# Kernel optimization log

Measured on AMD Instinct MI355X. Metric: run time of the kernel, lower is better.

Reference implementation:

```python
import jax, jax.numpy as jnp
import numpy as np
import math

LOG2PI = math.log(2.0 * math.pi)


def _gm_scale(m1, v1, m2, v2):
    # log-scale of product of two diagonal Gaussians (summed over last dim D)
    v1s = jnp.exp(2.0 * v1)
    v2s = jnp.exp(2.0 * v2)
    s = v1s + v2s
    ls = jnp.log(s)
    return (-0.5 * (LOG2PI + ls + (m1 - m2) ** 2 / s)).sum(-1)


def _gm_full(m1, v1, m2, v2):
    v1s = jnp.exp(2.0 * v1)
    v2s = jnp.exp(2.0 * v2)
    s = v1s + v2s
    ls = jnp.log(s)
    scale = (-0.5 * (LOG2PI + ls + (m1 - m2) ** 2 / s)).sum(-1)
    mu = (m1 * v2s + m2 * v1s) / s
    var = v1 + v2 - 0.5 * ls
    return scale, mu, var


def _child_part(cw, cm, cv, t_mu, t_var, side):
    # cw: (M,L,K); cm/cv: (M,L,K,D); t_mu/t_var: (L,L,L,C,D)
    if side == 'left':
        cm_b = cm[:, None, :, None, None, :, :]
        cv_b = cv[:, None, :, None, None, :, :]
        cw_b = cw[:, None, :, None, None, :]
    else:
        cm_b = cm[:, None, None, :, None, :, :]
        cv_b = cv[:, None, None, :, None, :, :]
        cw_b = cw[:, None, None, :, None, :]
    t_mu_b = t_mu[None, :, :, :, :, None, :]
    t_var_b = t_var[None, :, :, :, :, None, :]
    scale = _gm_scale(cm_b, cv_b, t_mu_b, t_var_b)  # (M,L,L,L,C,K)
    return jax.nn.logsumexp(scale + cw_b, axis=-1)  # (M,L,L,L,C)


def setup_inputs() -> dict:
    key = jax.random.key(0)
    ks = jax.random.split(key, 10)
    L, C, Ks, D = 5, 4, 4, 4
    n_leaves = 128
    N = 2 * n_leaves - 1  # complete binary tree, level order, leaves first
    f = jax.random.normal
    return {
        'state_weight': f(ks[0], (N, L, Ks), jnp.float32) * 0.5,
        'state_mu': f(ks[1], (N, L, Ks, D), jnp.float32) * 0.5,
        'state_var': f(ks[2], (N, L, Ks, D), jnp.float32) * 0.1,
        'trans_weight': f(ks[3], (L, L, L, C), jnp.float32) * 0.5,
        'trans_mu_p': f(ks[4], (L, L, L, C, D), jnp.float32) * 0.5,
        'trans_mu_lc': f(ks[5], (L, L, L, C, D), jnp.float32) * 0.5,
        'trans_mu_rc': f(ks[6], (L, L, L, C, D), jnp.float32) * 0.5,
        'trans_var_p': f(ks[7], (L, L, L, C, D), jnp.float32) * 0.1,
        'trans_var_lc': f(ks[8], (L, L, L, C, D), jnp.float32) * 0.1,
        'trans_var_rc': f(ks[9], (L, L, L, C, D), jnp.float32) * 0.1,
        'n_leaves': n_leaves,
    }


def reference(state_weight, state_mu, state_var, trans_weight, trans_mu_p,
              trans_mu_lc, trans_mu_rc, trans_var_p, trans_var_lc,
              trans_var_rc, n_leaves):
    L = trans_weight.shape[0]
    D = trans_mu_p.shape[-1]
    # inside pass over a complete binary tree, level by level
    w = state_weight[:n_leaves]      # (M,L,K)
    mu = state_mu[:n_leaves]         # (M,L,K,D)
    var = state_var[:n_leaves]
    off = n_leaves
    m = n_leaves // 2
    while m >= 1:
        left = _child_part(w[0::2], mu[0::2], var[0::2], trans_mu_lc, trans_var_lc, 'left')
        right = _child_part(w[1::2], mu[1::2], var[1::2], trans_mu_rc, trans_var_rc, 'right')
        cs = left + right + trans_weight[None]  # (m,L,L,L,C)
        sw = state_weight[off:off + m]          # (m,L,Ks)
        sm = state_mu[off:off + m]
        sv = state_var[off:off + m]
        sm_b = sm[:, :, None, None, :, None, :]   # (m,L,1,1,Ks,1,D)
        sv_b = sv[:, :, None, None, :, None, :]
        tp_mu = trans_mu_p[None, :, :, :, None, :, :]   # (1,L,L,L,1,C,D)
        tp_var = trans_var_p[None, :, :, :, None, :, :]
        scale, pmu, pvar = _gm_full(sm_b, sv_b, tp_mu, tp_var)  # (m,L,L,L,Ks,C)
        score = scale + cs[:, :, :, :, None, :] + sw[:, :, None, None, :, None]
        w = score.reshape(m, L, -1)  # K = L*L*Ks*C
        mu = jnp.broadcast_to(pmu, score.shape + (D,)).reshape(m, L, -1, D)
        var = jnp.broadcast_to(pvar, score.shape + (D,)).reshape(m, L, -1, D)
        off += m
        m //= 2
    return w[0], mu[0], var[0]
```

## Files before the change

### kernel.cpp

```cpp
#include <hip/hip_runtime.h>
#include <math.h>

#define L2PI4      7.3515082656373812f
#define HALF_L2PI4 3.6757541328186906f
#define LOG2E      1.4426950408889634f
#define LN2        0.6931471805599453f
#define C_HQ       0.7213475204444817f

__device__ __forceinline__ float frcp(float x)  { return __builtin_amdgcn_rcpf(x); }
__device__ __forceinline__ float frsq(float x)  { return __builtin_amdgcn_rsqf(x); }
__device__ __forceinline__ float flog2(float x) { return __builtin_amdgcn_logf(x); }
__device__ __forceinline__ float fexp2(float x) { return __builtin_amdgcn_exp2f(x); }

__global__ __launch_bounds__(256) void kL1(
    const float* __restrict__ sw, const float* __restrict__ smu,
    const float* __restrict__ svar,
    const float4* __restrict__ tmL4, const float4* __restrict__ tvL4,
    const float4* __restrict__ tmR4, const float4* __restrict__ tvR4,
    const float* __restrict__ tvarp, const float* __restrict__ tvarl,
    const float* __restrict__ tvarr,
    float* __restrict__ tveP, float* __restrict__ tveL, float* __restrict__ tveR,
    float* __restrict__ lr)
{
    int cn = blockIdx.x, side = cn & 1, tid = threadIdx.x;
    if (cn < 24) {
        int t = cn >> 3;
        int base = (cn & 7) * 250;
        const float* src = (t == 0) ? tvarp : (t == 1) ? tvarl : tvarr;
        float* dst       = (t == 0) ? tveP  : (t == 1) ? tveL  : tveR;
        for (int i = tid; i < 250; i += 256)
            dst[base + i] = __expf(2.f * src[base + i]);
    }
    __shared__ float s_cm[80], s_cve[80], s_cw2[20];
    if (tid < 80) {
        s_cm[tid]  = smu[cn * 80 + tid];
        s_cve[tid] = __expf(2.f * svar[cn * 80 + tid]);
        if (tid < 20) s_cw2[tid] = (sw[cn * 20 + tid] - HALF_L2PI4) * LOG2E;
    }
    __syncthreads();
    const float4* tm = side ? tmR4 : tmL4;
    const float4* tv = side ? tvR4 : tvL4;
    for (int e = tid; e < 500; e += 256) {
        int c = e & 3, r = e >> 2;
        int lo = r % 5, r2 = r / 5, lp = r2 % 5, lc2 = r2 / 5;
        int idx = side ? (((lp * 5 + lo) * 5 + lc2) * 4 + c)
                       : (((lp * 5 + lc2) * 5 + lo) * 4 + c);
        float4 tmo = tm[idx];
        float4 tvr = tv[idx];
        float4 tvo = make_float4(__expf(2.f * tvr.x), __expf(2.f * tvr.y),
                                 __expf(2.f * tvr.z), __expf(2.f * tvr.w));
        float vals[4];
        #pragma unroll
        for (int k = 0; k < 4; ++k) {
            int ci = (lc2 * 4 + k) * 4;
            float s0 = s_cve[ci+0] + tvo.x, s1 = s_cve[ci+1] + tvo.y;
            float s2 = s_cve[ci+2] + tvo.z, s3 = s_cve[ci+3] + tvo.w;
            float d0 = s_cm[ci+0] - tmo.x, d1 = s_cm[ci+1] - tmo.y;
            float d2 = s_cm[ci+2] - tmo.z, d3 = s_cm[ci+3] - tmo.w;
            float p01 = s0 * s1, p23 = s2 * s3;
            float q01 = fmaf(d0 * d0, s1, d1 * d1 * s0);
            float q23 = fmaf(d2 * d2, s3, d3 * d3 * s2);
            float P = p01 * p23;
            float Q = fmaf(q01, p23, q23 * p01);
            float rq = frsq(P);
            float QP = Q * rq * rq;
            vals[k] = fmaf(-0.5f, flog2(P), fmaf(-C_HQ, QP, s_cw2[lc2 * 4 + k]));
        }
        float M = fmaxf(fmaxf(vals[0], vals[1]), fmaxf(vals[2], vals[3]));
        float S = fexp2(vals[0]-M) + fexp2(vals[1]-M)
                + fexp2(vals[2]-M) + fexp2(vals[3]-M);
        lr[(size_t)cn * 500 + idx] = (M + flog2(S)) * LN2;
    }
}

__global__ __launch_bounds__(256) void kAB(
    const float* __restrict__ lrP, float* __restrict__ lrC,
    const float* __restrict__ sw, const float* __restrict__ smu,
    const float* __restrict__ svar, int childOff,
    const float* __restrict__ tw, const float4* __restrict__ tmp4,
    const float4* __restrict__ tep4,
    const float4* __restrict__ tmL4, const float4* __restrict__ tveL4,
    const float4* __restrict__ tmR4, const float4* __restrict__ tveR4,
    int log2m)
{
    int bid = blockIdx.x;
    int p = bid & ((1 << log2m) - 1), sl = bid >> log2m;
    int side = (sl >= 25) ? 1 : 0;
    int r0 = sl - side * 25;
    int lc = r0 / 5, lp = r0 - lc * 5;
    int tid = threadIdx.x, lane = tid & 63, wave = tid >> 6;
    int cn = 2 * p + side;
    int node = childOff + cn;

    __shared__ float  s_sm[16], s_sve[16], s_swl[4];
    __shared__ float4 s_fm[400], s_fv[400];
    __shared__ float  s_fw[400];
    __shared__ float4 s_tm[20], s_tv[20];
    __shared__ int    s_idx[20];

    if (tid < 16) {
        s_sm[tid]  = smu[node * 80 + lc * 16 + tid];
        s_sve[tid] = __expf(2.f * svar[node * 80 + lc * 16 + tid]);
        if (tid < 4) s_swl[tid] = sw[node * 20 + lc * 4 + tid];
    }
    {
        const float4* tmf  = side ? tmR4  : tmL4;
        const float4* tvef = side ? tveR4 : tveL4;
        if (tid >= 64 && tid < 84) {
            int o = tid - 64, lo = o >> 2, c = o & 3;
            int idx = side ? (((lp * 5 + lo) * 5 + lc) * 4 + c)
                           : (((lp * 5 + lc) * 5 + lo) * 4 + c);
            s_idx[o] = idx;
            s_tm[o]  = tmf[idx];
            s_tv[o]  = tvef[idx];
        }
    }
    __syncthreads();

    const float* lrL = lrP + (size_t)(2 * cn) * 500;
    const float* lrR = lrP + (size_t)(2 * cn + 1) * 500;

    for (int e = tid; e < 400; e += 256) {
        int c2 = e & 3, ks = (e >> 2) & 3, r = e >> 4;
        int t4 = (lc * 25 + r) * 4 + c2;
        float csv = lrL[t4] + lrR[t4] + tw[t4];
        float4 m2 = tmp4[t4], e2 = tep4[t4];
        float base2 = (csv + s_swl[ks] - L2PI4) * LOG2E;
        float v0 = s_sve[ks*4+0], v1 = s_sve[ks*4+1];
        float v2 = s_sve[ks*4+2], v3 = s_sve[ks*4+3];
        float m10 = s_sm[ks*4+0], m11 = s_sm[ks*4+1];
        float m12 = s_sm[ks*4+2], m13 = s_sm[ks*4+3];
        float s0 = v0 + e2.x, s1 = v1 + e2.y, s2 = v2 + e2.z, s3 = v3 + e2.w;
        float rs0 = frcp(s0), rs1 = frcp(s1), rs2 = frcp(s2), rs3 = frcp(s3);
        float d0 = m10 - m2.x, d1 = m11 - m2.y, d2 = m12 - m2.z, d3 = m13 - m2.w;
        float qs = fmaf(d0 * d0, rs0, fmaf(d1 * d1, rs1,
                   fmaf(d2 * d2, rs2, d3 * d3 * rs3)));
        float P = (s0 * s1) * (s2 * s3);
        float4 fm, fv;
        fm.x = fmaf(m10, e2.x, m2.x * v0) * rs0;  fv.x = v0 * e2.x * rs0;
        fm.y = fmaf(m11, e2.y, m2.y * v1) * rs1;  fv.y = v1 * e2.y * rs1;
        fm.z = fmaf(m12, e2.z, m2.z * v2) * rs2;  fv.z = v2 * e2.z * rs2;
        fm.w = fmaf(m13, e2.w, m2.w * v3) * rs3;  fv.w = v3 * e2.w * rs3;
        s_fm[e] = fm;
        s_fv[e] = fv;
        s_fw[e] = fmaf(-0.5f, flog2(P), fmaf(-C_HQ, qs, base2));
    }
    __syncthreads();

    float E[7], M;
    {
        float w[7];
        #pragma unroll
        for (int i = 0; i < 7; ++i) {
            int k = lane + (i << 6);
            int kc = k < 400 ? k : 0;
            w[i] = (k < 400) ? s_fw[kc] : -1e30f;
        }
        M = w[0];
        #pragma unroll
        for (int i = 1; i < 7; ++i) M = fmaxf(M, w[i]);
        #pragma unroll
        for (int s = 32; s; s >>= 1) M = fmaxf(M, __shfl_xor(M, s));
        #pragma unroll
        for (int i = 0; i < 7; ++i) E[i] = fexp2(w[i] - M);
    }

    size_t lrb = (size_t)cn * 500;
    #pragma unroll
    for (int j = 0; j < 5; ++j) {
        int o = wave + 4 * j;
        float4 tmo = s_tm[o], tvo = s_tv[o];
        float S = 0.f;
        #pragma unroll
        for (int i = 0; i < 7; ++i) {
            int k = lane + (i << 6);
            int kc = k < 400 ? k : 0;
            float4 fm = s_fm[kc], fv = s_fv[kc];
            float ss0 = fv.x + tvo.x, ss1 = fv.y + tvo.y;
            float ss2 = fv.z + tvo.z, ss3 = fv.w + tvo.w;
            float dd0 = fm.x - tmo.x, dd1 = fm.y - tmo.y;
            float dd2 = fm.z - tmo.z, dd3 = fm.w - tmo.w;
            float p01 = ss0 * ss1, p23 = ss2 * ss3;
            float q01 = fmaf(dd0 * dd0, ss1, dd1 * dd1 * ss0);
            float q23 = fmaf(dd2 * dd2, ss3, dd3 * dd3 * ss2);
            float P = p01 * p23;
            float Q = fmaf(q01, p23, q23 * p01);
            float rq = frsq(P);
            float QP = Q * rq * rq;
            S = fmaf(E[i] * rq, fexp2(-C_HQ * QP), S);
        }
        #pragma unroll
        for (int s = 32; s; s >>= 1) S += __shfl_xor(S, s);
        if (lane == 0) lrC[lrb + s_idx[o]] = (M + flog2(S)) * LN2;
    }
}

__global__ __launch_bounds__(256) void kFin(
    const float* __restrict__ lrC,
    const float* __restrict__ sw, const float* __restrict__ smu,
    const float* __restrict__ svar, int rootNode,
    const float* __restrict__ tw, const float4* __restrict__ tmp4,
    const float4* __restrict__ tvp4, const float4* __restrict__ tep4,
    float* __restrict__ outw, float4* __restrict__ outmu4,
    float4* __restrict__ outvar4)
{
    int e = blockIdx.x * 256 + threadIdx.x;
    if (e >= 2000) return;
    int c = e & 3, ks = (e >> 2) & 3, r = e >> 4;
    int lrc = r % 5, r2 = r / 5, llc = r2 % 5, lp = r2 / 5;
    int t4 = ((lp * 5 + llc) * 5 + lrc) * 4 + c;
    float csv = lrC[t4] + lrC[500 + t4] + tw[t4];
    float4 m2 = tmp4[t4], v2 = tvp4[t4], e2 = tep4[t4];
    int sb = rootNode * 80 + (lp * 4 + ks) * 4;
    float base = csv + sw[rootNode * 20 + lp * 4 + ks] - HALF_L2PI4;
    float scale = 0.f;
    float4 pmu, pvar;
    {
        float m1 = smu[sb+0], v1 = svar[sb+0], v1s = __expf(2.f * v1);
        float s = v1s + e2.x, rs = frcp(s), ls = flog2(s) * LN2, df = m1 - m2.x;
        scale += ls + df * df * rs;
        pmu.x = fmaf(m1, e2.x, m2.x * v1s) * rs; pvar.x = v1 + v2.x - 0.5f * ls;
    }
    {
        float m1 = smu[sb+1], v1 = svar[sb+1], v1s = __expf(2.f * v1);
        float s = v1s + e2.y, rs = frcp(s), ls = flog2(s) * LN2, df = m1 - m2.y;
        scale += ls + df * df * rs;
        pmu.y = fmaf(m1, e2.y, m2.y * v1s) * rs; pvar.y = v1 + v2.y - 0.5f * ls;
    }
    {
        float m1 = smu[sb+2], v1 = svar[sb+2], v1s = __expf(2.f * v1);
        float s = v1s + e2.z, rs = frcp(s), ls = flog2(s) * LN2, df = m1 - m2.z;
        scale += ls + df * df * rs;
        pmu.z = fmaf(m1, e2.z, m2.z * v1s) * rs; pvar.z = v1 + v2.z - 0.5f * ls;
    }
    {
        float m1 = smu[sb+3], v1 = svar[sb+3], v1s = __expf(2.f * v1);
        float s = v1s + e2.w, rs = frcp(s), ls = flog2(s) * LN2, df = m1 - m2.w;
        scale += ls + df * df * rs;
        pmu.w = fmaf(m1, e2.w, m2.w * v1s) * rs; pvar.w = v1 + v2.w - 0.5f * ls;
    }
    outw[e]    = fmaf(-0.5f, scale, base);
    outmu4[e]  = pmu;
    outvar4[e] = pvar;
}

extern "C" void kernel_launch(void* const* d_in, const int* in_sizes, int n_in,
                              void* d_out, int out_size, void* d_ws, size_t ws_size,
                              hipStream_t stream) {
    (void)in_sizes; (void)n_in; (void)out_size; (void)ws_size;
    const float* sw      = (const float*)d_in[0];
    const float* smu     = (const float*)d_in[1];
    const float* svar    = (const float*)d_in[2];
    const float* tw      = (const float*)d_in[3];
    const float* tmu_p   = (const float*)d_in[4];
    const float* tmu_lc  = (const float*)d_in[5];
    const float* tmu_rc  = (const float*)d_in[6];
    const float* tvar_p  = (const float*)d_in[7];
    const float* tvar_lc = (const float*)d_in[8];
    const float* tvar_rc = (const float*)d_in[9];

    float* ws   = (float*)d_ws;
    float* lrA  = ws;
    float* lrB  = lrA + 64000;
    float* tveP = lrB + 64000;
    float* tveL = tveP + 2000;
    float* tveR = tveL + 2000;
    float* out  = (float*)d_out;

    hipLaunchKernelGGL(kL1, dim3(128), dim3(256), 0, stream,
                       sw, smu, svar,
                       (const float4*)tmu_lc, (const float4*)tvar_lc,
                       (const float4*)tmu_rc, (const float4*)tvar_rc,
                       tvar_p, tvar_lc, tvar_rc,
                       tveP, tveL, tveR, lrA);

    const int childOffs[6] = {128, 192, 224, 240, 248, 252};
    float* lrP = lrA;
    float* lrC = lrB;
    int li = 0;
    for (int lg = 5; lg >= 0; --lg, ++li) {
        int m = 1 << lg;
        hipLaunchKernelGGL(kAB, dim3(50 * m), dim3(256), 0, stream,
                           lrP, lrC,
                           sw, smu, svar, childOffs[li],
                           tw, (const float4*)tmu_p, (const float4*)tveP,
                           (const float4*)tmu_lc, (const float4*)tveL,
                           (const float4*)tmu_rc, (const float4*)tveR,
                           lg);
        float* t = lrP; lrP = lrC; lrC = t;
    }
    hipLaunchKernelGGL(kFin, dim3(8), dim3(256), 0, stream,
                       lrP, sw, smu, svar, 254,
                       tw, (const float4*)tmu_p, (const float4*)tvar_p,
                       (const float4*)tveP,
                       out, (float4*)(out + 2000), (float4*)(out + 10000));
}
```

Baseline: 65.89 us.

## Fuse leaf-level lr computation into first tree level and final step into last

Removes the separate leaf kernel by having the first level kernel recompute both children's leaf log-responsibilities in shared memory. It also drops the precomputed exp(2*var) tables in favour of inline exponentials, and folds the final root kernel into the last level through an atomic last-block-done counter. Net effect: two fewer kernel launches plus a memset, in exchange for redundant leaf recomputation across the 25 lc/lp blocks that share each child pair and extra exp work.

Result: slower. 72.39 us (+9.9%).

```diff
diff --git a/kernel.cpp b/kernel.cpp
--- a/kernel.cpp
+++ b/kernel.cpp
@@ -12,119 +12,105 @@
 __device__ __forceinline__ float flog2(float x) { return __builtin_amdgcn_logf(x); }
 __device__ __forceinline__ float fexp2(float x) { return __builtin_amdgcn_exp2f(x); }
 
-__global__ __launch_bounds__(256) void kL1(
+__global__ __launch_bounds__(256) void kAB32(
     const float* __restrict__ sw, const float* __restrict__ smu,
     const float* __restrict__ svar,
+    const float* __restrict__ tw, const float4* __restrict__ tmp4,
+    const float4* __restrict__ tvp4,
     const float4* __restrict__ tmL4, const float4* __restrict__ tvL4,
     const float4* __restrict__ tmR4, const float4* __restrict__ tvR4,
-    const float* __restrict__ tvarp, const float* __restrict__ tvarl,
-    const float* __restrict__ tvarr,
-    float* __restrict__ tveP, float* __restrict__ tveL, float* __restrict__ tveR,
-    float* __restrict__ lr)
+    float* __restrict__ lrC)
 {
-    int cn = blockIdx.x, side = cn & 1, tid = threadIdx.x;
-    if (cn < 24) {
-        int t = cn >> 3;
-        int base = (cn & 7) * 250;
-        const float* src = (t == 0) ? tvarp : (t == 1) ? tvarl : tvarr;
-        float* dst       = (t == 0) ? tveP  : (t == 1) ? tveL  : tveR;
-        for (int i = tid; i < 250; i += 256)
-            dst[base + i] = __expf(2.f * src[base + i]);
-    }
-    __shared__ float s_cm[80], s_cve[80], s_cw2[20];
-    if (tid < 80) {
-        s_cm[tid]  = smu[cn * 80 + tid];
-        s_cve[tid] = __expf(2.f * svar[cn * 80 + tid]);
-        if (tid < 20) s_cw2[tid] = (sw[cn * 20 + tid] - HALF_L2PI4) * LOG2E;
-    }
-    __syncthreads();
-    const float4* tm = side ? tmR4 : tmL4;
-    const float4* tv = side ? tvR4 : tvL4;
-    for (int e = tid; e < 500; e += 256) {
-        int c = e & 3, r = e >> 2;
-        int lo = r % 5, r2 = r / 5, lp = r2 % 5, lc2 = r2 / 5;
-        int idx = side ? (((lp * 5 + lo) * 5 + lc2) * 4 + c)
-                       : (((lp * 5 + lc2) * 5 + lo) * 4 + c);
-        float4 tmo = tm[idx];
-        float4 tvr = tv[idx];
+    int bid = blockIdx.x;
+    int p = bid & 31, sl = bid >> 5;
+    int side = (sl >= 25) ? 1 : 0;
+    int r0 = sl - side * 25;
+    int lc = r0 / 5, lp = r0 - lc * 5;
+    int tid = threadIdx.x, lane = tid & 63, wave = tid >> 6;
+    int cn = 2 * p + side;
+    int node = 128 + cn;
+
+    __shared__ float  s_lm[160], s_lve[160], s_lw2[40];
+    __shared__ float  s_lr[200];
+    __shared__ float  s_sm[16], s_sve[16], s_swl[4];
+    __shared__ float4 s_fm[400], s_fv[400];
+    __shared__ float  s_fw[400];
+    __shared__ float4 s_tm[20], s_tv[20];
+    __shared__ int    s_idx[20];
+
+    if (tid < 160) {
+        int which = tid >= 80, i = tid - which * 80;
+        int nl = 2 * cn + which;
+        s_lm[tid]  = smu[nl * 80 + i];
+        s_lve[tid] = __expf(2.f * svar[nl * 80 + i]);
+    } else if (tid < 200) {
+        int t = tid - 160, which = t >= 20, i = t - which * 20;
+        int nl = 2 * cn + which;
+        s_lw2[t] = (sw[nl * 20 + i] - HALF_L2PI4) * LOG2E;
+    } else if (tid < 216) {
+        int i = tid - 200;
+        s_sm[i]  = smu[node * 80 + lc * 16 + i];
+        s_sve[i] = __expf(2.f * svar[node * 80 + lc * 16 + i]);
+    } else if (tid < 220) {
+        s_swl[tid - 216] = sw[node * 20 + lc * 4 + (tid - 216)];
+    } else if (tid < 240) {
+        int o = tid - 220, lo = o >> 2, c = o & 3;
+        int idx = side ? (((lp * 5 + lo) * 5 + lc) * 4 + c)
+                       : (((lp * 5 + lc) * 5 + lo) * 4 + c);
+        s_idx[o] = idx;
+        const float4* tmf = side ? tmR4 : tmL4;
+        const float4* tvf = side ? tvR4 : tvL4;
+        s_tm[o] = tmf[idx];
+        float4 tvr = tvf[idx];
+        s_tv[o] = make_float4(__expf(2.f * tvr.x), __expf(2.f * tvr.y),
+                              __expf(2.f * tvr.z), __expf(2.f * tvr.w));
+    }
+    __syncthreads();
+
+    for (int t = tid; t < 200; t += 256) {
+        int which = t >= 100, q = t - which * 100;
+        int r = q >> 2, c2 = q & 3;
+        int llc = r / 5, lrc = r - llc * 5;
+        int t4 = (lc * 25 + r) * 4 + c2;
+        int lab = which ? lrc : llc;
+        float4 tm  = (which ? tmR4 : tmL4)[t4];
+        float4 tvr = (which ? tvR4 : tvL4)[t4];
         float4 tvo = make_float4(__expf(2.f * tvr.x), __expf(2.f * tvr.y),
                                  __expf(2.f * tvr.z), __expf(2.f * tvr.w));
+        int sb = which * 80 + lab * 16;
         float vals[4];
         #pragma unroll
         for (int k = 0; k < 4; ++k) {
-            int ci = (lc2 * 4 + k) * 4;
-            float s0 = s_cve[ci+0] + tvo.x, s1 = s_cve[ci+1] + tvo.y;
-            float s2 = s_cve[ci+2] + tvo.z, s3 = s_cve[ci+3] + tvo.w;
-            float d0 = s_cm[ci+0] - tmo.x, d1 = s_cm[ci+1] - tmo.y;
-            float d2 = s_cm[ci+2] - tmo.z, d3 = s_cm[ci+3] - tmo.w;
+            int ci = sb + k * 4;
+            float s0 = s_lve[ci+0] + tvo.x, s1 = s_lve[ci+1] + tvo.y;
+            float s2 = s_lve[ci+2] + tvo.z, s3 = s_lve[ci+3] + tvo.w;
+            float d0 = s_lm[ci+0] - tm.x, d1 = s_lm[ci+1] - tm.y;
+            float d2 = s_lm[ci+2] - tm.z, d3 = s_lm[ci+3] - tm.w;
             float p01 = s0 * s1, p23 = s2 * s3;
             float q01 = fmaf(d0 * d0, s1, d1 * d1 * s0);
             float q23 = fmaf(d2 * d2, s3, d3 * d3 * s2);
             float P = p01 * p23;
             float Q = fmaf(q01, p23, q23 * p01);
             float rq = frsq(P);
-            float QP = Q * rq * rq;
-            vals[k] = fmaf(-0.5f, flog2(P), fmaf(-C_HQ, QP, s_cw2[lc2 * 4 + k]));
+            vals[k] = fmaf(-0.5f, flog2(P),
+                           fmaf(-C_HQ, Q * rq * rq, s_lw2[which * 20 + lab * 4 + k]));
         }
         float M = fmaxf(fmaxf(vals[0], vals[1]), fmaxf(vals[2], vals[3]));
         float S = fexp2(vals[0]-M) + fexp2(vals[1]-M)
                 + fexp2(vals[2]-M) + fexp2(vals[3]-M);
-        lr[(size_t)cn * 500 + idx] = (M + flog2(S)) * LN2;
-    }
-}
-
-__global__ __launch_bounds__(256) void kAB(
-    const float* __restrict__ lrP, float* __restrict__ lrC,
-    const float* __restrict__ sw, const float* __restrict__ smu,
-    const float* __restrict__ svar, int childOff,
-    const float* __restrict__ tw, const float4* __restrict__ tmp4,
-    const float4* __restrict__ tep4,
-    const float4* __restrict__ tmL4, const float4* __restrict__ tveL4,
-    const float4* __restrict__ tmR4, const float4* __restrict__ tveR4,
-    int log2m)
-{
-    int bid = blockIdx.x;
-    int p = bid & ((1 << log2m) - 1), sl = bid >> log2m;
-    int side = (sl >= 25) ? 1 : 0;
-    int r0 = sl - side * 25;
-    int lc = r0 / 5, lp = r0 - lc * 5;
-    int tid = threadIdx.x, lane = tid & 63, wave = tid >> 6;
-    int cn = 2 * p + side;
-    int node = childOff + cn;
-
-    __shared__ float  s_sm[16], s_sve[16], s_swl[4];
-    __shared__ float4 s_fm[400], s_fv[400];
-    __shared__ float  s_fw[400];
-    __shared__ float4 s_tm[20], s_tv[20];
-    __shared__ int    s_idx[20];
-
-    if (tid < 16) {
-        s_sm[tid]  = smu[node * 80 + lc * 16 + tid];
-        s_sve[tid] = __expf(2.f * svar[node * 80 + lc * 16 + tid]);
-        if (tid < 4) s_swl[tid] = sw[node * 20 + lc * 4 + tid];
-    }
-    {
-        const float4* tmf  = side ? tmR4  : tmL4;
-        const float4* tvef = side ? tveR4 : tveL4;
-        if (tid >= 64 && tid < 84) {
-            int o = tid - 64, lo = o >> 2, c = o & 3;
-            int idx = side ? (((lp * 5 + lo) * 5 + lc) * 4 + c)
-                           : (((lp * 5 + lc) * 5 + lo) * 4 + c);
-            s_idx[o] = idx;
-            s_tm[o]  = tmf[idx];
-            s_tv[o]  = tvef[idx];
-        }
-    }
-    __syncthreads();
-
-    const float* lrL = lrP + (size_t)(2 * cn) * 500;
-    const float* lrR = lrP + (size_t)(2 * cn + 1) * 500;
+        s_lr[t] = (M + flog2(S)) * LN2;
+    }
+    __syncthreads();
 
     for (int e = tid; e < 400; e += 256) {
         int c2 = e & 3, ks = (e >> 2) & 3, r = e >> 4;
+        int q = r * 4 + c2;
         int t4 = (lc * 25 + r) * 4 + c2;
-        float csv = lrL[t4] + lrR[t4] + tw[t4];
-        float4 m2 = tmp4[t4], e2 = tep4[t4];
+        float csv = s_lr[q] + s_lr[100 + q] + tw[t4];
+        float4 m2 = tmp4[t4];
+        float4 vr = tvp4[t4];
+        float4 e2 = make_float4(__expf(2.f * vr.x), __expf(2.f * vr.y),
+                                __expf(2.f * vr.z), __expf(2.f * vr.w));
         float base2 = (csv + s_swl[ks] - L2PI4) * LOG2E;
         float v0 = s_sve[ks*4+0], v1 = s_sve[ks*4+1];
         float v2 = s_sve[ks*4+2], v3 = s_sve[ks*4+3];
@@ -153,8 +139,7 @@
         #pragma unroll
         for (int i = 0; i < 7; ++i) {
             int k = lane + (i << 6);
-            int kc = k < 400 ? k : 0;
-            w[i] = (k < 400) ? s_fw[kc] : -1e30f;
+            w[i] = (k < 400) ? s_fw[k] : -1e30f;
         }
         M = w[0];
         #pragma unroll
@@ -164,7 +149,6 @@
         #pragma unroll
         for (int i = 0; i < 7; ++i) E[i] = fexp2(w[i] - M);
     }
-
     size_t lrb = (size_t)cn * 500;
     #pragma unroll
     for (int j = 0; j < 5; ++j) {
@@ -186,8 +170,7 @@
             float P = p01 * p23;
             float Q = fmaf(q01, p23, q23 * p01);
             float rq = frsq(P);
-            float QP = Q * rq * rq;
-            S = fmaf(E[i] * rq, fexp2(-C_HQ * QP), S);
+            S = fmaf(E[i] * rq, fexp2(-C_HQ * (Q * rq * rq)), S);
         }
         #pragma unroll
         for (int s = 32; s; s >>= 1) S += __shfl_xor(S, s);
@@ -195,53 +178,183 @@
     }
 }
 
-__global__ __launch_bounds__(256) void kFin(
-    const float* __restrict__ lrC,
+__global__ __launch_bounds__(256) void kAB(
+    const float* __restrict__ lrP, float* __restrict__ lrC,
     const float* __restrict__ sw, const float* __restrict__ smu,
-    const float* __restrict__ svar, int rootNode,
+    const float* __restrict__ svar, int childOff,
     const float* __restrict__ tw, const float4* __restrict__ tmp4,
-    const float4* __restrict__ tvp4, const float4* __restrict__ tep4,
-    float* __restrict__ outw, float4* __restrict__ outmu4,
-    float4* __restrict__ outvar4)
+    const float4* __restrict__ tvp4,
+    const float4* __restrict__ tmL4, const float4* __restrict__ tvL4,
+    const float4* __restrict__ tmR4, const float4* __restrict__ tvR4,
+    int log2m, int doFin, unsigned* __restrict__ cnt, float* __restrict__ out)
 {
-    int e = blockIdx.x * 256 + threadIdx.x;
-    if (e >= 2000) return;
-    int c = e & 3, ks = (e >> 2) & 3, r = e >> 4;
-    int lrc = r % 5, r2 = r / 5, llc = r2 % 5, lp = r2 / 5;
-    int t4 = ((lp * 5 + llc) * 5 + lrc) * 4 + c;
-    float csv = lrC[t4] + lrC[500 + t4] + tw[t4];
-    float4 m2 = tmp4[t4], v2 = tvp4[t4], e2 = tep4[t4];
-    int sb = rootNode * 80 + (lp * 4 + ks) * 4;
-    float base = csv + sw[rootNode * 20 + lp * 4 + ks] - HALF_L2PI4;
-    float scale = 0.f;
-    float4 pmu, pvar;
+    int bid = blockIdx.x;
+    int p = bid & ((1 << log2m) - 1), sl = bid >> log2m;
+    int side = (sl >= 25) ? 1 : 0;
+    int r0 = sl - side * 25;
+    int lc = r0 / 5, lp = r0 - lc * 5;
+    int tid = threadIdx.x, lane = tid & 63, wave = tid >> 6;
+    int cn = 2 * p + side;
+    int node = childOff + cn;
+
+    __shared__ float  s_sm[16], s_sve[16], s_swl[4];
+    __shared__ float4 s_fm[400], s_fv[400];
+    __shared__ float  s_fw[400];
+    __shared__ float4 s_tm[20], s_tv[20];
+    __shared__ int    s_idx[20];
+    __shared__ int    s_last;
+
+    if (tid < 16) {
+        s_sm[tid]  = smu[node * 80 + lc * 16 + tid];
+        s_sve[tid] = __expf(2.f * svar[node * 80 + lc * 16 + tid]);
+        if (tid < 4) s_swl[tid] = sw[node * 20 + lc * 4 + tid];
+    }
+    if (tid >= 64 && tid < 84) {
+        int o = tid - 64, lo = o >> 2, c = o & 3;
+        int idx = side ? (((lp * 5 + lo) * 5 + lc) * 4 + c)
+                       : (((lp * 5 + lc) * 5 + lo) * 4 + c);
+        s_idx[o] = idx;
+        const float4* tmf = side ? tmR4 : tmL4;
+        const float4* tvf = side ? tvR4 : tvL4;
+        s_tm[o] = tmf[idx];
+        float4 tvr = tvf[idx];
+        s_tv[o] = make_float4(__expf(2.f * tvr.x), __expf(2.f * tvr.y),
+                              __expf(2.f * tvr.z), __expf(2.f * tvr.w));
+    }
+    __syncthreads();
+
+    const float* lrL = lrP + (size_t)(2 * cn) * 500;
+    const float* lrR = lrP + (size_t)(2 * cn + 1) * 500;
+
+    for (int e = tid; e < 400; e += 256) {
+        int c2 = e & 3, ks = (e >> 2) & 3, r = e >> 4;
+        int t4 = (lc * 25 + r) * 4 + c2;
+        float csv = lrL[t4] + lrR[t4] + tw[t4];
+        float4 m2 = tmp4[t4];
+        float4 vr = tvp4[t4];
+        float4 e2 = make_float4(__expf(2.f * vr.x), __expf(2.f * vr.y),
+                                __expf(2.f * vr.z), __expf(2.f * vr.w));
+        float base2 = (csv + s_swl[ks] - L2PI4) * LOG2E;
+        float v0 = s_sve[ks*4+0], v1 = s_sve[ks*4+1];
+        float v2 = s_sve[ks*4+2], v3 = s_sve[ks*4+3];
+        float m10 = s_sm[ks*4+0], m11 = s_sm[ks*4+1];
+        float m12 = s_sm[ks*4+2], m13 = s_sm[ks*4+3];
+        float s0 = v0 + e2.x, s1 = v1 + e2.y, s2 = v2 + e2.z, s3 = v3 + e2.w;
+        float rs0 = frcp(s0), rs1 = frcp(s1), rs2 = frcp(s2), rs3 = frcp(s3);
+        float d0 = m10 - m2.x, d1 = m11 - m2.y, d2 = m12 - m2.z, d3 = m13 - m2.w;
+        float qs = fmaf(d0 * d0, rs0, fmaf(d1 * d1, rs1,
+                   fmaf(d2 * d2, rs2, d3 * d3 * rs3)));
+        float P = (s0 * s1) * (s2 * s3);
+        float4 fm, fv;
+        fm.x = fmaf(m10, e2.x, m2.x * v0) * rs0;  fv.x = v0 * e2.x * rs0;
+        fm.y = fmaf(m11, e2.y, m2.y * v1) * rs1;  fv.y = v1 * e2.y * rs1;
+        fm.z = fmaf(m12, e2.z, m2.z * v2) * rs2;  fv.z = v2 * e2.z * rs2;
+        fm.w = fmaf(m13, e2.w, m2.w * v3) * rs3;  fv.w = v3 * e2.w * rs3;
+        s_fm[e] = fm;
+        s_fv[e] = fv;
+        s_fw[e] = fmaf(-0.5f, flog2(P), fmaf(-C_HQ, qs, base2));
+    }
+    __syncthreads();
+
+    float E[7], M;
     {
-        float m1 = smu[sb+0], v1 = svar[sb+0], v1s = __expf(2.f * v1);
-        float s = v1s + e2.x, rs = frcp(s), ls = flog2(s) * LN2, df = m1 - m2.x;
-        scale += ls + df * df * rs;
-        pmu.x = fmaf(m1, e2.x, m2.x * v1s) * rs; pvar.x = v1 + v2.x - 0.5f * ls;
-    }
-    {
-        float m1 = smu[sb+1], v1 = svar[sb+1], v1s = __expf(2.f * v1);
-        float s = v1s + e2.y, rs = frcp(s), ls = flog2(s) * LN2, df = m1 - m2.y;
-        scale += ls + df * df * rs;
-        pmu.y = fmaf(m1, e2.y, m2.y * v1s) * rs; pvar.y = v1 + v2.y - 0.5f * ls;
-    }
-    {
-        float m1 = smu[sb+2], v1 = svar[sb+2], v1s = __expf(2.f * v1);
-        float s = v1s + e2.z, rs = frcp(s), ls = flog2(s) * LN2, df = m1 - m2.z;
-        scale += ls + df * df * rs;
-        pmu.z = fmaf(m1, e2.z, m2.z * v1s) * rs; pvar.z = v1 + v2.z - 0.5f * ls;
-    }
-    {
-        float m1 = smu[sb+3], v1 = svar[sb+3], v1s = __expf(2.f * v1);
-        float s = v1s + e2.w, rs = frcp(s), ls = flog2(s) * LN2, df = m1 - m2.w;
-        scale += ls + df * df * rs;
-        pmu.w = fmaf(m1, e2.w, m2.w * v1s) * rs; pvar.w = v1 + v2.w - 0.5f * ls;
-    }
-    outw[e]    = fmaf(-0.5f, scale, base);
-    outmu4[e]  = pmu;
-    outvar4[e] = pvar;
+        float w[7];
+        #pragma unroll
+        for (int i = 0; i < 7; ++i) {
+            int k = lane + (i << 6);
+            w[i] = (k < 400) ? s_fw[k] : -1e30f;
+        }
+        M = w[0];
+        #pragma unroll
+        for (int i = 1; i < 7; ++i) M = fmaxf(M, w[i]);
+        #pragma unroll
+        for (int s = 32; s; s >>= 1) M = fmaxf(M, __shfl_xor(M, s));
+        #pragma unroll
+        for (int i = 0; i < 7; ++i) E[i] = fexp2(w[i] - M);
+    }
+
+    size_t lrb = (size_t)cn * 500;
+    #pragma unroll
+    for (int j = 0; j < 5; ++j) {
+        int o = wave + 4 * j;
+        float4 tmo = s_tm[o], tvo = s_tv[o];
+        float S = 0.f;
+        #pragma unroll
+        for (int i = 0; i < 7; ++i) {
+            int k = lane + (i << 6);
+            int kc = k < 400 ? k : 0;
+            float4 fm = s_fm[kc], fv = s_fv[kc];
+            float ss0 = fv.x + tvo.x, ss1 = fv.y + tvo.y;
+            float ss2 = fv.z + tvo.z, ss3 = fv.w + tvo.w;
+            float dd0 = fm.x - tmo.x, dd1 = fm.y - tmo.y;
+            float dd2 = fm.z - tmo.z, dd3 = fm.w - tmo.w;
+            float p01 = ss0 * ss1, p23 = ss2 * ss3;
+            float q01 = fmaf(dd0 * dd0, ss1, dd1 * dd1 * ss0);
+            float q23 = fmaf(dd2 * dd2, ss3, dd3 * dd3 * ss2);
+            float P = p01 * p23;
+            float Q = fmaf(q01, p23, q23 * p01);
+            float rq = frsq(P);
+            S = fmaf(E[i] * rq, fexp2(-C_HQ * (Q * rq * rq)), S);
+        }
+        #pragma unroll
+        for (int s = 32; s; s >>= 1) S += __shfl_xor(S, s);
+        if (lane == 0) lrC[lrb + s_idx[o]] = (M + flog2(S)) * LN2;
+    }
+
+    if (!doFin) return;
+    __syncthreads();
+    if (tid == 0) {
+        __builtin_amdgcn_fence(__ATOMIC_RELEASE, "agent");
+        unsigned old = __hip_atomic_fetch_add(cnt, 1u, __ATOMIC_RELAXED,
+                                              __HIP_MEMORY_SCOPE_AGENT);
+        s_last = (old == 49u);
+    }
+    __syncthreads();
+    if (!s_last) return;
+    __builtin_amdgcn_fence(__ATOMIC_ACQUIRE, "agent");
+
+    float4* outmu4  = (float4*)(out + 2000);
+    float4* outvar4 = (float4*)(out + 10000);
+    for (int e = tid; e < 2000; e += 256) {
+        int c = e & 3, ks = (e >> 2) & 3, r = e >> 4;
+        int lrc = r % 5, r2 = r / 5, llc = r2 % 5, lp2 = r2 / 5;
+        int t4 = ((lp2 * 5 + llc) * 5 + lrc) * 4 + c;
+        float csv = lrC[t4] + lrC[500 + t4] + tw[t4];
+        float4 m2 = tmp4[t4], v2 = tvp4[t4];
+        float4 e2 = make_float4(__expf(2.f * v2.x), __expf(2.f * v2.y),
+                                __expf(2.f * v2.z), __expf(2.f * v2.w));
+        int sb = 254 * 80 + (lp2 * 4 + ks) * 4;
+        float base = csv + sw[254 * 20 + lp2 * 4 + ks] - HALF_L2PI4;
+        float scale = 0.f;
+        float4 pmu, pvar;
+        {
+            float m1 = smu[sb+0], v1 = svar[sb+0], v1s = __expf(2.f * v1);
+            float s = v1s + e2.x, rs = frcp(s), ls = flog2(s) * LN2, df = m1 - m2.x;
+            scale += ls + df * df * rs;
+            pmu.x = fmaf(m1, e2.x, m2.x * v1s) * rs; pvar.x = v1 + v2.x - 0.5f * ls;
+        }
+        {
+            float m1 = smu[sb+1], v1 = svar[sb+1], v1s = __expf(2.f * v1);
+            float s = v1s + e2.y, rs = frcp(s), ls = flog2(s) * LN2, df = m1 - m2.y;
+            scale += ls + df * df * rs;
+            pmu.y = fmaf(m1, e2.y, m2.y * v1s) * rs; pvar.y = v1 + v2.y - 0.5f * ls;
+        }
+        {
+            float m1 = smu[sb+2], v1 = svar[sb+2], v1s = __expf(2.f * v1);
+            float s = v1s + e2.z, rs = frcp(s), ls = flog2(s) * LN2, df = m1 - m2.z;
+            scale += ls + df * df * rs;
+            pmu.z = fmaf(m1, e2.z, m2.z * v1s) * rs; pvar.z = v1 + v2.z - 0.5f * ls;
+        }
+        {
+            float m1 = smu[sb+3], v1 = svar[sb+3], v1s = __expf(2.f * v1);
+            float s = v1s + e2.w, rs = frcp(s), ls = flog2(s) * LN2, df = m1 - m2.w;
+            scale += ls + df * df * rs;
+            pmu.w = fmaf(m1, e2.w, m2.w * v1s) * rs; pvar.w = v1 + v2.w - 0.5f * ls;
+        }
+        out[e]     = fmaf(-0.5f, scale, base);
+        outmu4[e]  = pmu;
+        outvar4[e] = pvar;
+    }
 }
 
 extern "C" void kernel_launch(void* const* d_in, const int* in_sizes, int n_in,
@@ -262,36 +375,32 @@
     float* ws   = (float*)d_ws;
     float* lrA  = ws;
     float* lrB  = lrA + 64000;
-    float* tveP = lrB + 64000;
-    float* tveL = tveP + 2000;
-    float* tveR = tveL + 2000;
+    unsigned* cnt = (unsigned*)(lrB + 64000);
     float* out  = (float*)d_out;
 
-    hipLaunchKernelGGL(kL1, dim3(128), dim3(256), 0, stream,
-                       sw, smu, svar,
+    hipMemsetAsync(cnt, 0, sizeof(unsigned), stream);
+
+    hipLaunchKernelGGL(kAB32, dim3(1600), dim3(256), 0, stream,
+                       sw, smu, svar, tw,
+                       (const float4*)tmu_p, (const float4*)tvar_p,
                        (const float4*)tmu_lc, (const float4*)tvar_lc,
                        (const float4*)tmu_rc, (const float4*)tvar_rc,
-                       tvar_p, tvar_lc, tvar_rc,
-                       tveP, tveL, tveR, lrA);
-
-    const int childOffs[6] = {128, 192, 224, 240, 248, 252};
+                       lrA);
+
+    const int childOffs[5] = {192, 224, 240, 248, 252};
     float* lrP = lrA;
     float* lrC = lrB;
     int li = 0;
-    for (int lg = 5; lg >= 0; --lg, ++li) {
+    for (int lg = 4; lg >= 0; --lg, ++li) {
         int m = 1 << lg;
+        int fin = (m == 1);
         hipLaunchKernelGGL(kAB, dim3(50 * m), dim3(256), 0, stream,
                            lrP, lrC,
                            sw, smu, svar, childOffs[li],
-                           tw, (const float4*)tmu_p, (const float4*)tveP,
-                           (const float4*)tmu_lc, (const float4*)tveL,
-                           (const float4*)tmu_rc, (const float4*)tveR,
-                           lg);
+                           tw, (const float4*)tmu_p, (const float4*)tvar_p,
+                           (const float4*)tmu_lc, (const float4*)tvar_lc,
+                           (const float4*)tmu_rc, (const float4*)tvar_rc,
+                           lg, fin, cnt, out);
         float* t = lrP; lrP = lrC; lrC = t;
     }
-    hipLaunchKernelGGL(kFin, dim3(8), dim3(256), 0, stream,
-                       lrP, sw, smu, svar, 254,
-                       tw, (const float4*)tmu_p, (const float4*)tvar_p,
-                       (const float4*)tveP,
-                       out, (float4*)(out + 2000), (float4*)(out + 10000));
 }
```
